# Kernel optimization log

Measured on AMD Instinct MI355X. Metric: run time of the kernel, lower is better.

The kernel has to match this reference:

```python
import jax, jax.numpy as jnp
import numpy as np

NC, ND, B, K = 10000, 1000000, 8192, 64
EMB = 16
CH_DENSE, DEV_DENSE = 16, 20
CAT_MAX = [100, 4, 50, 200, 500, 1000, 300]  # lang, plat, os, country, carrier, brand, plat_os
H1, H2, ATTN_H = 64, 64, 84
IN1 = CH_DENSE + EMB        # 32  (channel dense + channel_id emb)
IN2 = DEV_DENSE + 7 * EMB   # 132 (device dense + 7 cat embs)


def setup_inputs() -> dict:
    key = jax.random.key(0)
    ks = jax.random.split(key, 32)
    def nrm(k, shape, s=0.05):
        return jax.random.normal(k, shape, dtype=jnp.float32) * s
    inp = {}
    inp["channel_dense"] = nrm(ks[0], (NC, CH_DENSE), 1.0)
    inp["device_dense"] = nrm(ks[1], (ND, DEV_DENSE), 1.0)
    inp["channel_id_emb"] = nrm(ks[2], (NC, EMB))
    names = ["lang_emb", "plat_emb", "os_emb", "country_emb", "carrier_emb", "brand_emb", "plat_os_emb"]
    for i, (n, m) in enumerate(zip(names, CAT_MAX)):
        inp[n] = nrm(ks[3 + i], (m, EMB))
    inp["W_agg"] = nrm(ks[10], (IN2, H2));  inp["b_agg"] = jnp.zeros((H2,), jnp.float32)
    inp["W_self"] = nrm(ks[11], (IN1, H1)); inp["b_self"] = jnp.zeros((H1,), jnp.float32)
    inp["W_attn"] = nrm(ks[12], (H2 + IN1, ATTN_H)); inp["b_attn"] = jnp.zeros((ATTN_H,), jnp.float32)
    inp["W_attn2"] = nrm(ks[13], (ATTN_H, 1)); inp["b_attn2"] = jnp.zeros((1,), jnp.float32)
    inp["channel_ids"] = jax.random.randint(ks[14], (NC,), 0, NC)
    cat_cols = [jax.random.randint(ks[15 + i], (ND,), 0, m) for i, m in enumerate(CAT_MAX)]
    inp["device_cat"] = jnp.stack(cat_cols, axis=1)  # [ND, 7]
    inp["vertices"] = jax.random.randint(ks[22], (B,), 0, NC)
    inp["bot_neibrs"] = jax.random.randint(ks[23], (B, K), 0, ND)
    inp["normal_neibrs"] = jax.random.randint(ks[24], (B, K), 0, ND)
    inp["bot_counts"] = jax.random.randint(ks[25], (B,), 1, K + 1)
    inp["normal_counts"] = jax.random.randint(ks[26], (B,), 1, K + 1)
    return inp


def reference(channel_dense, device_dense, channel_id_emb, lang_emb, plat_emb, os_emb,
              country_emb, carrier_emb, brand_emb, plat_os_emb,
              W_agg, b_agg, W_self, b_self, W_attn, b_attn, W_attn2, b_attn2,
              channel_ids, device_cat, vertices, bot_neibrs, normal_neibrs,
              bot_counts, normal_counts):
    cat_tables = [lang_emb, plat_emb, os_emb, country_emb, carrier_emb, brand_emb, plat_os_emb]
    # channel self features: dense cols + channel_id embedding  -> [B, IN1]
    ch_v = jnp.concatenate([channel_dense[vertices],
                            channel_id_emb[channel_ids[vertices]]], axis=1)

    def agg(neibrs, counts):
        # gather neighbor device features, embed categoricals, masked mean, linear (Mean_agg)
        dense = device_dense[neibrs]                                   # [B, K, DEV_DENSE]
        cats = device_cat[neibrs]                                      # [B, K, 7]
        embs = jnp.concatenate([t[cats[..., i]] for i, t in enumerate(cat_tables)], axis=-1)
        feats = jnp.concatenate([dense, embs], axis=-1)                # [B, K, IN2]
        mask = (jnp.arange(K)[None, :] < counts[:, None]).astype(feats.dtype)
        mean = jnp.sum(feats * mask[..., None], axis=1) / jnp.maximum(counts, 1).astype(feats.dtype)[:, None]
        return mean @ W_agg + b_agg                                    # [B, H2]

    bots = agg(bot_neibrs, bot_counts)
    normal = agg(normal_neibrs, normal_counts)

    def score(h):
        # attention MLP on concat(aggregated feats, channel self feats)
        return jax.nn.relu(jnp.concatenate([h, ch_v], axis=1) @ W_attn + b_attn) @ W_attn2 + b_attn2

    a = jax.nn.softmax(jnp.concatenate([score(bots), score(normal)], axis=1), axis=1)  # [B, 2]
    gcn = a[:, 0:1] * bots + a[:, 1:2] * normal                        # convex combination [B, H2]
    # Msg_out: relu(concat(agg_out, linear(self)))
    return jax.nn.relu(jnp.concatenate([gcn, ch_v @ W_self + b_self], axis=1))  # [B, H2+H1]
```

## Files before the change

### kernel.cpp

```cpp
#include <hip/hip_runtime.h>

#define BATCH 8192
#define KNB   64
#define EMB   16
#define CHD   16
#define DVD   20
#define H1    64
#define H2    64
#define AH    84
#define IN1   32
#define IN2   132

#define RB 32
#define VB 16

typedef float vf4 __attribute__((ext_vector_type(4)));

__global__ __launch_bounds__(128, 4) void gconv_gather(
    const float* __restrict__ device_dense,
    const float* __restrict__ t0, const float* __restrict__ t1,
    const float* __restrict__ t2, const float* __restrict__ t3,
    const float* __restrict__ t4, const float* __restrict__ t5,
    const float* __restrict__ t6,
    const int* __restrict__ device_cat,
    const int* __restrict__ bot_neibrs,
    const int* __restrict__ normal_neibrs,
    const int* __restrict__ bot_counts,
    const int* __restrict__ normal_counts,
    float* __restrict__ fsum_ws)
{
    const int t    = threadIdx.x;
    const int w    = t >> 6;
    const int L    = t & 63;
    const int kk   = L >> 5;
    const int slot = L & 31;
    const int item = blockIdx.x * 2 + w;
    const int v    = item >> 1;

    __shared__ alignas(16) int ofs[2][KNB][8];

    int cnt = (item & 1) ? normal_counts[v] : bot_counts[v];
    cnt = cnt < 1 ? 1 : (cnt > KNB ? KNB : cnt);
    cnt = __builtin_amdgcn_readfirstlane(cnt);

    {
        const int* nb = (item & 1) ? normal_neibrs : bot_neibrs;
        int n = 0;
        if (L < cnt) n = nb[v * KNB + L];
        const long cb = (long)n * 7;
        const int4 cA = *(const int4*)(device_cat + cb);
        const int4 cB = *(const int4*)(device_cat + cb + 3);
        *(int4*)&ofs[w][L][0] = make_int4(n * DVD, cA.x * EMB, cA.y * EMB, cA.z * EMB);
        *(int4*)&ofs[w][L][4] = make_int4(cA.w * EMB, cB.y * EMB, cB.z * EMB, cB.w * EMB);
    }
    __asm__ volatile("s_waitcnt lgkmcnt(0)" ::: "memory");
    __builtin_amdgcn_sched_barrier(0);

    const float* P;
    int oIdx, col, feat;
    if (slot < 5) {
        P = device_dense; oIdx = 0; col = slot * 4; feat = slot * 4;
    } else {
        const int e  = slot - 5;
        const int tb = e >> 2;
        const int q  = e & 3;
        oIdx = 1 + tb; col = 4 * q; feat = 20 + 16 * tb + 4 * q;
        switch (tb) {
            case 0: P = t0; break;
            case 1: P = t1; break;
            case 2: P = t2; break;
            case 3: P = t3; break;
            case 4: P = t4; break;
            case 5: P = t5; break;
            default: P = t6; break;
        }
    }

    vf4 acc = {0.f, 0.f, 0.f, 0.f};
    const int passes = (cnt + 1) >> 1;
    for (int pc = 0; pc < passes; pc += 8) {
        int o[8];
        #pragma unroll
        for (int j = 0; j < 8; ++j)
            o[j] = ofs[w][2 * (pc + j) + kk][oIdx];
        vf4 val[8];
        #pragma unroll
        for (int j = 0; j < 8; ++j) {
            const float* ap = P + o[j] + col;
            asm volatile("global_load_dwordx4 %0, %1, off"
                         : "=v"(val[j]) : "v"(ap) : "memory");
        }
        asm volatile("s_waitcnt vmcnt(0)" ::: "memory");
        __builtin_amdgcn_sched_barrier(0);
        #pragma unroll
        for (int j = 0; j < 8; ++j) {
            const float m = (2 * (pc + j) + kk < cnt) ? 1.f : 0.f;
            acc[0] = fmaf(m, val[j][0], acc[0]);
            acc[1] = fmaf(m, val[j][1], acc[1]);
            acc[2] = fmaf(m, val[j][2], acc[2]);
            acc[3] = fmaf(m, val[j][3], acc[3]);
        }
    }

    acc[0] += __shfl_xor(acc[0], 32, 64);
    acc[1] += __shfl_xor(acc[1], 32, 64);
    acc[2] += __shfl_xor(acc[2], 32, 64);
    acc[3] += __shfl_xor(acc[3], 32, 64);

    {
        const int o32 = ofs[w][L][7];
        const float4 vx = *(const float4*)(t6 + o32 + 12);
        const float m = (L < cnt) ? 1.f : 0.f;
        float4 ax = make_float4(m * vx.x, m * vx.y, m * vx.z, m * vx.w);
        #pragma unroll
        for (int off = 1; off < 64; off <<= 1) {
            ax.x += __shfl_xor(ax.x, off, 64);
            ax.y += __shfl_xor(ax.y, off, 64);
            ax.z += __shfl_xor(ax.z, off, 64);
            ax.w += __shfl_xor(ax.w, off, 64);
        }
        if (L == 0)
            *(float4*)(fsum_ws + (size_t)item * IN2 + 128) = ax;
    }

    if (L < 32)
        *(float4*)(fsum_ws + (size_t)item * IN2 + feat) =
            make_float4(acc[0], acc[1], acc[2], acc[3]);
}

__global__ __launch_bounds__(256) void gconv_dense(
    const float* __restrict__ channel_dense,
    const float* __restrict__ channel_id_emb,
    const float* __restrict__ W_agg,  const float* __restrict__ b_agg,
    const float* __restrict__ W_self, const float* __restrict__ b_self,
    const float* __restrict__ W_attn, const float* __restrict__ b_attn,
    const float* __restrict__ W_attn2,
    const int* __restrict__ channel_ids,
    const int* __restrict__ vertices,
    const int* __restrict__ bot_counts,
    const int* __restrict__ normal_counts,
    const float* __restrict__ fsum_ws,
    float* __restrict__ out)
{
    const int blk = blockIdx.x;
    const int b0  = blk * RB;
    const int v0  = blk * VB;
    const int t   = threadIdx.x;

    __shared__ alignas(16) float fs[RB][IN2];
    __shared__ alignas(16) float chvs[VB][IN1];
    __shared__ alignas(16) float hs[RB][H2];
    __shared__ float u_lds[AH][RB + 1];
    __shared__ float sarr[RB];
    __shared__ float cinv[RB];

    for (int idx = t; idx < RB * IN2 / 4; idx += 256) {
        const float4 vv = *(const float4*)(fsum_ws + (size_t)b0 * IN2 + idx * 4);
        *(float4*)&((float*)fs)[idx * 4] = vv;
    }
    if (t < RB) {
        const int b = b0 + t;
        const int v = b >> 1;
        int c = (b & 1) ? normal_counts[v] : bot_counts[v];
        c = (c > KNB) ? KNB : ((c < 1) ? 1 : c);
        cinv[t] = 1.0f / (float)c;
    }
    if (t < 128) {
        const int vx = t >> 3, q = t & 7;
        const int vert = vertices[v0 + vx];
        const float* src = (q < 4)
            ? channel_dense  + (size_t)vert * CHD + q * 4
            : channel_id_emb + (size_t)channel_ids[vert] * EMB + (q - 4) * 4;
        *(float4*)&chvs[vx][q * 4] = *(const float4*)src;
    }
    __syncthreads();

    {
        const int w = t >> 6, lane = t & 63;
        const int r0 = w * 8;
        float acc[8] = {0.f, 0.f, 0.f, 0.f, 0.f, 0.f, 0.f, 0.f};
        #pragma unroll 4
        for (int f = 0; f < IN2; ++f) {
            const float wv = W_agg[f * H2 + lane];
            #pragma unroll
            for (int r = 0; r < 8; ++r)
                acc[r] = fmaf(fs[r0 + r][f], wv, acc[r]);
        }
        const float bb = b_agg[lane];
        #pragma unroll
        for (int r = 0; r < 8; ++r)
            hs[r0 + r][lane] = fmaf(acc[r], cinv[r0 + r], bb);
    }
    __syncthreads();

    if (t < 2 * AH) {
        const int rg = (t >= AH) ? 1 : 0;
        const int aa = t - AH * rg;
        const int r0 = rg * 16;
        float acc[16];
        #pragma unroll
        for (int r = 0; r < 16; ++r) acc[r] = 0.f;
        #pragma unroll 2
        for (int f = 0; f < H2; ++f) {
            const float wv = W_attn[f * AH + aa];
            #pragma unroll
            for (int r = 0; r < 16; ++r)
                acc[r] = fmaf(hs[r0 + r][f], wv, acc[r]);
        }
        #pragma unroll 2
        for (int f = 0; f < IN1; ++f) {
            const float wv = W_attn[(H2 + f) * AH + aa];
            #pragma unroll
            for (int r = 0; r < 16; ++r)
                acc[r] = fmaf(chvs[(r0 + r) >> 1][f], wv, acc[r]);
        }
        const float ba = b_attn[aa], w2 = W_attn2[aa];
        #pragma unroll
        for (int r = 0; r < 16; ++r)
            u_lds[aa][r0 + r] = fmaxf(acc[r] + ba, 0.f) * w2;
    }
    __syncthreads();

    if (t < RB) {
        float s = 0.f;
        #pragma unroll 4
        for (int aa = 0; aa < AH; ++aa) s += u_lds[aa][t];
        sarr[t] = s;
    }
    __syncthreads();

    {
        const int vl = t >> 4;
        const int c8 = (t & 15) * 8;
        const float s0 = sarr[2 * vl], s1 = sarr[2 * vl + 1];
        const float mm = fmaxf(s0, s1);
        const float e0 = __expf(s0 - mm), e1 = __expf(s1 - mm);
        const float rs = 1.0f / (e0 + e1);
        const float a0 = e0 * rs, a1 = e1 * rs;
        float o[8];
        if (c8 < H2) {
            #pragma unroll
            for (int c = 0; c < 8; ++c)
                o[c] = fmaxf(a0 * hs[2 * vl][c8 + c] + a1 * hs[2 * vl + 1][c8 + c], 0.f);
        } else {
            const int cs = c8 - H2;
            float accS[8];
            #pragma unroll
            for (int c = 0; c < 8; ++c) accS[c] = b_self[cs + c];
            #pragma unroll 4
            for (int f = 0; f < IN1; ++f) {
                const float xv = chvs[vl][f];
                const float4 wa = *(const float4*)(W_self + f * H1 + cs);
                const float4 wb = *(const float4*)(W_self + f * H1 + cs + 4);
                accS[0] = fmaf(xv, wa.x, accS[0]);
                accS[1] = fmaf(xv, wa.y, accS[1]);
                accS[2] = fmaf(xv, wa.z, accS[2]);
                accS[3] = fmaf(xv, wa.w, accS[3]);
                accS[4] = fmaf(xv, wb.x, accS[4]);
                accS[5] = fmaf(xv, wb.y, accS[5]);
                accS[6] = fmaf(xv, wb.z, accS[6]);
                accS[7] = fmaf(xv, wb.w, accS[7]);
            }
            #pragma unroll
            for (int c = 0; c < 8; ++c) o[c] = fmaxf(accS[c], 0.f);
        }
        float4* op = (float4*)(out + (size_t)(v0 + vl) * (H1 + H2) + c8);
        op[0] = make_float4(o[0], o[1], o[2], o[3]);
        op[1] = make_float4(o[4], o[5], o[6], o[7]);
    }
}

extern "C" void kernel_launch(void* const* d_in, const int* in_sizes, int n_in,
                              void* d_out, int out_size, void* d_ws, size_t ws_size,
                              hipStream_t stream) {
    const float* channel_dense  = (const float*)d_in[0];
    const float* device_dense   = (const float*)d_in[1];
    const float* channel_id_emb = (const float*)d_in[2];
    const float* lang_emb       = (const float*)d_in[3];
    const float* plat_emb       = (const float*)d_in[4];
    const float* os_emb         = (const float*)d_in[5];
    const float* country_emb    = (const float*)d_in[6];
    const float* carrier_emb    = (const float*)d_in[7];
    const float* brand_emb      = (const float*)d_in[8];
    const float* plat_os_emb    = (const float*)d_in[9];
    const float* W_agg          = (const float*)d_in[10];
    const float* b_agg          = (const float*)d_in[11];
    const float* W_self         = (const float*)d_in[12];
    const float* b_self         = (const float*)d_in[13];
    const float* W_attn         = (const float*)d_in[14];
    const float* b_attn         = (const float*)d_in[15];
    const float* W_attn2        = (const float*)d_in[16];
    const int* channel_ids   = (const int*)d_in[18];
    const int* device_cat    = (const int*)d_in[19];
    const int* vertices      = (const int*)d_in[20];
    const int* bot_neibrs    = (const int*)d_in[21];
    const int* normal_neibrs = (const int*)d_in[22];
    const int* bot_counts    = (const int*)d_in[23];
    const int* normal_counts = (const int*)d_in[24];

    float* fsum_ws = (float*)d_ws;
    float* out     = (float*)d_out;

    gconv_gather<<<dim3(2 * BATCH / 2), dim3(128), 0, stream>>>(
        device_dense, lang_emb, plat_emb, os_emb, country_emb, carrier_emb,
        brand_emb, plat_os_emb, device_cat, bot_neibrs, normal_neibrs,
        bot_counts, normal_counts, fsum_ws);

    gconv_dense<<<dim3(2 * BATCH / RB), dim3(256), 0, stream>>>(
        channel_dense, channel_id_emb, W_agg, b_agg, W_self, b_self,
        W_attn, b_attn, W_attn2, channel_ids, vertices,
        bot_counts, normal_counts, fsum_ws, out);
}
```

Measured before the change: 72.09 us.

## Stage small embedding tables in LDS and software-pipeline neighbor index loads across items

The gather kernel now handles four items per wave with double-buffered offset tables in shared memory. It prefetches the next item's neighbor IDs and categorical codes while accumulating the current item. The three smallest embedding tables (lang, plat, os) are copied into LDS once per block and read from there instead of global memory, and the lanes are remapped so global gathers and LDS reads are split between slots. This trades fewer blocks and more per-block LDS setup for hiding index-load latency and cutting global traffic for the small tables.

New measurement: 75.90 us. +5.3%, slower.

```diff
diff --git a/kernel.cpp b/kernel.cpp
--- a/kernel.cpp
+++ b/kernel.cpp
@@ -13,6 +13,7 @@
 
 #define RB 32
 #define VB 16
+#define NIW 4
 
 typedef float vf4 __attribute__((ext_vector_type(4)));
 
@@ -34,98 +35,151 @@
     const int L    = t & 63;
     const int kk   = L >> 5;
     const int slot = L & 31;
-    const int item = blockIdx.x * 2 + w;
-    const int v    = item >> 1;
-
-    __shared__ alignas(16) int ofs[2][KNB][8];
-
-    int cnt = (item & 1) ? normal_counts[v] : bot_counts[v];
-    cnt = cnt < 1 ? 1 : (cnt > KNB ? KNB : cnt);
-    cnt = __builtin_amdgcn_readfirstlane(cnt);
+
+    __shared__ alignas(16) float lds_tab[2464];
+    __shared__ alignas(16) int   ofs[2][2][KNB][8];
+
+    for (int i = t; i < 616; i += 128) {
+        float4 vsrc;
+        if (i < 400)      vsrc = ((const float4*)t0)[i];
+        else if (i < 416) vsrc = ((const float4*)t1)[i - 400];
+        else              vsrc = ((const float4*)t2)[i - 416];
+        ((float4*)lds_tab)[i] = vsrc;
+    }
+
+    const int base = (blockIdx.x * 2 + w) * NIW;
+
+    int cnts[NIW];
+    #pragma unroll
+    for (int i = 0; i < NIW; ++i) {
+        const int itn = base + i;
+        int c = (itn & 1) ? normal_counts[itn >> 1] : bot_counts[itn >> 1];
+        cnts[i] = c < 1 ? 1 : (c > KNB ? KNB : c);
+    }
 
     {
-        const int* nb = (item & 1) ? normal_neibrs : bot_neibrs;
-        int n = 0;
-        if (L < cnt) n = nb[v * KNB + L];
+        const int itn = base;
+        const int* nbp = (itn & 1) ? normal_neibrs : bot_neibrs;
+        const int n = (L < cnts[0]) ? nbp[(itn >> 1) * KNB + L] : 0;
         const long cb = (long)n * 7;
         const int4 cA = *(const int4*)(device_cat + cb);
         const int4 cB = *(const int4*)(device_cat + cb + 3);
-        *(int4*)&ofs[w][L][0] = make_int4(n * DVD, cA.x * EMB, cA.y * EMB, cA.z * EMB);
-        *(int4*)&ofs[w][L][4] = make_int4(cA.w * EMB, cB.y * EMB, cB.z * EMB, cB.w * EMB);
-    }
-    __asm__ volatile("s_waitcnt lgkmcnt(0)" ::: "memory");
-    __builtin_amdgcn_sched_barrier(0);
-
-    const float* P;
+        *(int4*)&ofs[w][0][L][0] = make_int4(n * DVD, cA.x * EMB,
+                                             1600 + cA.y * EMB, 1664 + cA.z * EMB);
+        *(int4*)&ofs[w][0][L][4] = make_int4(cA.w * EMB, cB.y * EMB,
+                                             cB.z * EMB, cB.w * EMB);
+    }
+    __syncthreads();
+
+    const float* P = device_dense;
     int oIdx, col, feat;
-    if (slot < 5) {
-        P = device_dense; oIdx = 0; col = slot * 4; feat = slot * 4;
-    } else {
-        const int e  = slot - 5;
-        const int tb = e >> 2;
-        const int q  = e & 3;
-        oIdx = 1 + tb; col = 4 * q; feat = 20 + 16 * tb + 4 * q;
-        switch (tb) {
-            case 0: P = t0; break;
-            case 1: P = t1; break;
-            case 2: P = t2; break;
-            case 3: P = t3; break;
-            case 4: P = t4; break;
-            case 5: P = t5; break;
-            default: P = t6; break;
-        }
-    }
-
-    vf4 acc = {0.f, 0.f, 0.f, 0.f};
-    const int passes = (cnt + 1) >> 1;
-    for (int pc = 0; pc < passes; pc += 8) {
-        int o[8];
-        #pragma unroll
-        for (int j = 0; j < 8; ++j)
-            o[j] = ofs[w][2 * (pc + j) + kk][oIdx];
-        vf4 val[8];
-        #pragma unroll
-        for (int j = 0; j < 8; ++j) {
-            const float* ap = P + o[j] + col;
-            asm volatile("global_load_dwordx4 %0, %1, off"
-                         : "=v"(val[j]) : "v"(ap) : "memory");
-        }
-        asm volatile("s_waitcnt vmcnt(0)" ::: "memory");
-        __builtin_amdgcn_sched_barrier(0);
-        #pragma unroll
-        for (int j = 0; j < 8; ++j) {
-            const float m = (2 * (pc + j) + kk < cnt) ? 1.f : 0.f;
-            acc[0] = fmaf(m, val[j][0], acc[0]);
-            acc[1] = fmaf(m, val[j][1], acc[1]);
-            acc[2] = fmaf(m, val[j][2], acc[2]);
-            acc[3] = fmaf(m, val[j][3], acc[3]);
-        }
-    }
-
-    acc[0] += __shfl_xor(acc[0], 32, 64);
-    acc[1] += __shfl_xor(acc[1], 32, 64);
-    acc[2] += __shfl_xor(acc[2], 32, 64);
-    acc[3] += __shfl_xor(acc[3], 32, 64);
-
-    {
-        const int o32 = ofs[w][L][7];
-        const float4 vx = *(const float4*)(t6 + o32 + 12);
-        const float m = (L < cnt) ? 1.f : 0.f;
-        float4 ax = make_float4(m * vx.x, m * vx.y, m * vx.z, m * vx.w);
-        #pragma unroll
-        for (int off = 1; off < 64; off <<= 1) {
-            ax.x += __shfl_xor(ax.x, off, 64);
-            ax.y += __shfl_xor(ax.y, off, 64);
-            ax.z += __shfl_xor(ax.z, off, 64);
-            ax.w += __shfl_xor(ax.w, off, 64);
-        }
-        if (L == 0)
-            *(float4*)(fsum_ws + (size_t)item * IN2 + 128) = ax;
-    }
-
-    if (L < 32)
-        *(float4*)(fsum_ws + (size_t)item * IN2 + feat) =
-            make_float4(acc[0], acc[1], acc[2], acc[3]);
+    if (slot < 5)       { P = device_dense; oIdx = 0; col = 4 * slot;        feat = col; }
+    else if (slot < 9)  { P = t3; oIdx = 4; col = 4 * (slot - 5);  feat = 68  + col; }
+    else if (slot < 13) { P = t4; oIdx = 5; col = 4 * (slot - 9);  feat = 84  + col; }
+    else if (slot < 17) { P = t5; oIdx = 6; col = 4 * (slot - 13); feat = 100 + col; }
+    else if (slot < 21) { P = t6; oIdx = 7; col = 4 * (slot - 17); feat = 116 + col; }
+    else if (slot < 25) { oIdx = 1; col = 4 * (slot - 21); feat = 20 + col; }
+    else if (slot < 29) { oIdx = 3; col = 4 * (slot - 25); feat = 52 + col; }
+    else                { oIdx = 2; col = 4 * (slot - 29); feat = 36 + col; }
+    const bool isG = (slot < 21);
+
+    #pragma unroll
+    for (int i = 0; i < NIW; ++i) {
+        const int cnt = cnts[i];
+        const int buf = i & 1;
+        const int item = base + i;
+
+        int nNext = 0;
+        if (i + 1 < NIW) {
+            const int itn = item + 1;
+            const int* nbp = (itn & 1) ? normal_neibrs : bot_neibrs;
+            nNext = (L < cnts[i + 1]) ? nbp[(itn >> 1) * KNB + L] : 0;
+            __builtin_amdgcn_sched_barrier(0);
+        }
+
+        vf4 acc  = {0.f, 0.f, 0.f, 0.f};
+        vf4 acc2 = {0.f, 0.f, 0.f, 0.f};
+        int4 cA = make_int4(0, 0, 0, 0), cB = make_int4(0, 0, 0, 0);
+
+        const int nchunks = (((cnt + 1) >> 1) + 7) >> 3;
+        for (int c = 0; c < nchunks; ++c) {
+            const int pc = c * 8;
+            int o[8];
+            #pragma unroll
+            for (int j = 0; j < 8; ++j)
+                o[j] = ofs[w][buf][2 * (pc + j) + kk][oIdx];
+            if (isG) {
+                vf4 val[8];
+                #pragma unroll
+                for (int j = 0; j < 8; ++j) {
+                    const float* ap = P + o[j] + col;
+                    asm volatile("global_load_dwordx4 %0, %1, off"
+                                 : "=v"(val[j]) : "v"(ap) : "memory");
+                }
+                asm volatile("s_waitcnt vmcnt(0)" ::: "memory");
+                __builtin_amdgcn_sched_barrier(0);
+                #pragma unroll
+                for (int j = 0; j < 8; ++j) {
+                    const float m = (2 * (pc + j) + kk < cnt) ? 1.f : 0.f;
+                    acc[0] = fmaf(m, val[j][0], acc[0]);
+                    acc[1] = fmaf(m, val[j][1], acc[1]);
+                    acc[2] = fmaf(m, val[j][2], acc[2]);
+                    acc[3] = fmaf(m, val[j][3], acc[3]);
+                }
+            } else {
+                #pragma unroll
+                for (int j = 0; j < 8; ++j) {
+                    const float m = (2 * (pc + j) + kk < cnt) ? 1.f : 0.f;
+                    const float4 lv = *(const float4*)&lds_tab[o[j] + col];
+                    acc[0] = fmaf(m, lv.x, acc[0]);
+                    acc[1] = fmaf(m, lv.y, acc[1]);
+                    acc[2] = fmaf(m, lv.z, acc[2]);
+                    acc[3] = fmaf(m, lv.w, acc[3]);
+                    if (slot == 29) {
+                        const float4 l2 = *(const float4*)&lds_tab[o[j] + 12];
+                        acc2[0] = fmaf(m, l2.x, acc2[0]);
+                        acc2[1] = fmaf(m, l2.y, acc2[1]);
+                        acc2[2] = fmaf(m, l2.z, acc2[2]);
+                        acc2[3] = fmaf(m, l2.w, acc2[3]);
+                    }
+                }
+            }
+            if (c == 0 && i + 1 < NIW) {
+                const long cb = (long)nNext * 7;
+                cA = *(const int4*)(device_cat + cb);
+                cB = *(const int4*)(device_cat + cb + 3);
+                __builtin_amdgcn_sched_barrier(0);
+            }
+        }
+
+        acc[0] += __shfl_xor(acc[0], 32, 64);
+        acc[1] += __shfl_xor(acc[1], 32, 64);
+        acc[2] += __shfl_xor(acc[2], 32, 64);
+        acc[3] += __shfl_xor(acc[3], 32, 64);
+        if (slot == 29) {
+            acc2[0] += __shfl_xor(acc2[0], 32, 64);
+            acc2[1] += __shfl_xor(acc2[1], 32, 64);
+            acc2[2] += __shfl_xor(acc2[2], 32, 64);
+            acc2[3] += __shfl_xor(acc2[3], 32, 64);
+        }
+
+        if (L < 32)
+            *(float4*)(fsum_ws + (size_t)item * IN2 + feat) =
+                make_float4(acc[0], acc[1], acc[2], acc[3]);
+        if (L == 29)
+            *(float4*)(fsum_ws + (size_t)item * IN2 + 48) =
+                make_float4(acc2[0], acc2[1], acc2[2], acc2[3]);
+
+        if (i + 1 < NIW) {
+            asm volatile("s_waitcnt vmcnt(0)" ::: "memory");
+            *(int4*)&ofs[w][buf ^ 1][L][0] = make_int4(nNext * DVD, cA.x * EMB,
+                                                 1600 + cA.y * EMB, 1664 + cA.z * EMB);
+            *(int4*)&ofs[w][buf ^ 1][L][4] = make_int4(cA.w * EMB, cB.y * EMB,
+                                                 cB.z * EMB, cB.w * EMB);
+            asm volatile("s_waitcnt lgkmcnt(0)" ::: "memory");
+            __builtin_amdgcn_sched_barrier(0);
+        }
+    }
 }
 
 __global__ __launch_bounds__(256) void gconv_dense(
@@ -301,7 +355,7 @@
     float* fsum_ws = (float*)d_ws;
     float* out     = (float*)d_out;
 
-    gconv_gather<<<dim3(2 * BATCH / 2), dim3(128), 0, stream>>>(
+    gconv_gather<<<dim3(2 * BATCH / (2 * NIW)), dim3(128), 0, stream>>>(
         device_dense, lang_emb, plat_emb, os_emb, country_emb, carrier_emb,
         brand_emb, plat_os_emb, device_cat, bot_neibrs, normal_neibrs,
         bot_counts, normal_counts, fsum_ws);
```
